# Kernel optimization log

Measured on AMD Instinct MI355X. Metric: run time of the kernel, lower is better.

The kernel has to match this reference:

```python
import jax, jax.numpy as jnp
import numpy as np
import itertools


def _comb_indices(F, k):
    # Flattened combination indices: for each of C(F,k) combinations, its k
    # member feature ids, concatenated. Row i of the original one-hot crmatrix
    # has a single 1 at column idx[i], so x @ crmatrix^T == gather by idx.
    return np.fromiter(itertools.chain(*itertools.combinations(range(F), k)),
                       dtype=np.int32)


def setup_inputs() -> dict:
    key = jax.random.key(0)
    x = jax.random.normal(key, (32, 4096, 32), dtype=jnp.float32)  # [B, T, F]
    return {"x": x, "k": 2}


def reference(x, k):
    F = x.shape[2]
    idx = jnp.asarray(_comb_indices(F, k))          # [ncr] = [k * C(F,k)]
    # Faithful to K.dot(x, crmatrix) with one-hot crmatrix: a feature gather.
    return jnp.take(x, idx, axis=2)                 # [B, T, ncr]
```

## Files before the change

### kernel.cpp

```cpp
#include <hip/hip_runtime.h>


#define FDIM 32
#define NCR 992
#define G_PER_ROW 248
#define TROWS 16
#define BLOCK 256

typedef float f32x4 __attribute__((ext_vector_type(4)));

__global__ __launch_bounds__(BLOCK)
void comb_gather_kernel(const float* __restrict__ x,
                        float* __restrict__ out,
                        int nrows) {
    const int g    = threadIdx.x;
    const int row0 = blockIdx.x * TROWS;
    if (g >= G_PER_ROW) return;

    int feat[4];
    {
        const int c0 = 2 * g;
        float s = sqrtf(3969.0f - 8.0f * (float)c0);
        int i0 = (int)((63.0f - s) * 0.5f);
        if (i0 < 0) i0 = 0;
        int st0  = (i0 * (63 - i0)) >> 1;
        int stn0 = ((i0 + 1) * (62 - i0)) >> 1;
        if (stn0 <= c0) { i0++; st0 = stn0; stn0 = ((i0 + 1) * (62 - i0)) >> 1; }
        else if (st0 > c0) { i0--; stn0 = st0; st0 = (i0 * (63 - i0)) >> 1; }
        feat[0] = i0;
        feat[1] = c0 - st0 + i0 + 1;
        const int c1 = c0 + 1;
        int i1 = i0, st1 = st0;
        if (stn0 <= c1) { i1 = i0 + 1; st1 = stn0; }
        feat[2] = i1;
        feat[3] = c1 - st1 + i1 + 1;
    }

    const float* rp = x + (size_t)row0 * FDIM;
    f32x4* outp = reinterpret_cast<f32x4*>(out + (size_t)row0 * NCR) + g;

    if (row0 + TROWS <= nrows) {
        #pragma unroll
        for (int r = 0; r < TROWS; ++r) {
            const float* rowp = rp + r * FDIM;
            f32x4 v;
            v.x = rowp[feat[0]];
            v.y = rowp[feat[1]];
            v.z = rowp[feat[2]];
            v.w = rowp[feat[3]];
            __builtin_nontemporal_store(v, outp);
            outp += NCR / 4;
        }
    } else {
        for (int r = 0; r < nrows - row0; ++r) {
            const float* rowp = rp + r * FDIM;
            f32x4 v;
            v.x = rowp[feat[0]];
            v.y = rowp[feat[1]];
            v.z = rowp[feat[2]];
            v.w = rowp[feat[3]];
            __builtin_nontemporal_store(v, outp);
            outp += NCR / 4;
        }
    }
}

extern "C" void kernel_launch(void* const* d_in, const int* in_sizes, int n_in,
                              void* d_out, int out_size, void* d_ws, size_t ws_size,
                              hipStream_t stream) {
    const float* x  = (const float*)d_in[0];
    float* out      = (float*)d_out;
    int nrows = in_sizes[0] / FDIM;
    int grid  = (nrows + TROWS - 1) / TROWS;
    hipLaunchKernelGGL(comb_gather_kernel, dim3(grid), dim3(BLOCK), 0, stream,
                       x, out, nrows);
}
```

Measured before the change: 103.6 us.

## Use persistent grid-stride blocks with an upfront prefetch of input rows

```diff
diff --git a/kernel.cpp b/kernel.cpp
--- a/kernel.cpp
+++ b/kernel.cpp
@@ -4,22 +4,32 @@
 #define FDIM 32
 #define NCR 992
 #define G_PER_ROW 248
-#define TROWS 16
 #define BLOCK 256
+#define GRID 2048
 
 typedef float f32x4 __attribute__((ext_vector_type(4)));
 
-__global__ __launch_bounds__(BLOCK)
+__global__ __launch_bounds__(BLOCK, 8)
 void comb_gather_kernel(const float* __restrict__ x,
                         float* __restrict__ out,
                         int nrows) {
-    const int g    = threadIdx.x;
-    const int row0 = blockIdx.x * TROWS;
-    if (g >= G_PER_ROW) return;
+    const int tid = threadIdx.x;
+    const int b   = blockIdx.x;
+
+    {
+        const int r = tid;
+        size_t row = (size_t)b + (size_t)r * GRID;
+        if (tid < 64 && row < (size_t)nrows) {
+            float w = x[row * FDIM];
+            asm volatile("" :: "v"(w));
+        }
+    }
+
+    if (tid >= G_PER_ROW) return;
 
     int feat[4];
     {
-        const int c0 = 2 * g;
+        const int c0 = 2 * tid;
         float s = sqrtf(3969.0f - 8.0f * (float)c0);
         int i0 = (int)((63.0f - s) * 0.5f);
         if (i0 < 0) i0 = 0;
@@ -36,32 +46,23 @@
         feat[3] = c1 - st1 + i1 + 1;
     }
 
-    const float* rp = x + (size_t)row0 * FDIM;
-    f32x4* outp = reinterpret_cast<f32x4*>(out + (size_t)row0 * NCR) + g;
+    const float* rowp = x + (size_t)b * FDIM;
+    f32x4*       outp = reinterpret_cast<f32x4*>(out + (size_t)b * NCR) + tid;
+    const size_t xstep = (size_t)GRID * FDIM;
+    const size_t ostep = (size_t)GRID * (NCR / 4);
 
-    if (row0 + TROWS <= nrows) {
-        #pragma unroll
-        for (int r = 0; r < TROWS; ++r) {
-            const float* rowp = rp + r * FDIM;
-            f32x4 v;
-            v.x = rowp[feat[0]];
-            v.y = rowp[feat[1]];
-            v.z = rowp[feat[2]];
-            v.w = rowp[feat[3]];
-            __builtin_nontemporal_store(v, outp);
-            outp += NCR / 4;
-        }
-    } else {
-        for (int r = 0; r < nrows - row0; ++r) {
-            const float* rowp = rp + r * FDIM;
-            f32x4 v;
-            v.x = rowp[feat[0]];
-            v.y = rowp[feat[1]];
-            v.z = rowp[feat[2]];
-            v.w = rowp[feat[3]];
-            __builtin_nontemporal_store(v, outp);
-            outp += NCR / 4;
-        }
+    const int iters = (nrows - b + GRID - 1) / GRID;
+
+    #pragma unroll 4
+    for (int r = 0; r < iters; ++r) {
+        f32x4 v;
+        v.x = rowp[feat[0]];
+        v.y = rowp[feat[1]];
+        v.z = rowp[feat[2]];
+        v.w = rowp[feat[3]];
+        __builtin_nontemporal_store(v, outp);
+        rowp += xstep;
+        outp += ostep;
     }
 }
 
@@ -71,7 +72,6 @@
     const float* x  = (const float*)d_in[0];
     float* out      = (float*)d_out;
     int nrows = in_sizes[0] / FDIM;
-    int grid  = (nrows + TROWS - 1) / TROWS;
-    hipLaunchKernelGGL(comb_gather_kernel, dim3(grid), dim3(BLOCK), 0, stream,
+    hipLaunchKernelGGL(comb_gather_kernel, dim3(GRID), dim3(BLOCK), 0, stream,
                        x, out, nrows);
 }
```

New measurement: 103.5 us. No clear change (-0.1%).
